# Performance work log

Measured on AMD Instinct MI355X. Metric: run time of the kernel, lower is better.

## Reference

```python
import jax, jax.numpy as jnp
import numpy as np

B, T, N, C, H = 32, 50, 1024, 128, 64


def setup_inputs() -> dict:
    key = jax.random.key(0)
    ks = jax.random.split(key, 5)
    s_ih = 1.0 / np.sqrt(H)
    return {
        "chars": jax.random.normal(ks[0], (B, T, N, C), dtype=jnp.float32),
        "W_ih": jax.random.uniform(ks[1], (3 * H, C), minval=-s_ih, maxval=s_ih, dtype=jnp.float32),
        "W_hh": jax.random.uniform(ks[2], (3 * H, H), minval=-s_ih, maxval=s_ih, dtype=jnp.float32),
        "b_ih": jax.random.uniform(ks[3], (3 * H,), minval=-s_ih, maxval=s_ih, dtype=jnp.float32),
        "b_hh": jax.random.uniform(ks[4], (3 * H,), minval=-s_ih, maxval=s_ih, dtype=jnp.float32),
    }


def _gru_scan(chars, W_ih, W_hh, b_ih, b_hh):
    b, t, n, c = chars.shape
    h_dim = W_hh.shape[1]
    # (B,T,N,C) -> (T, B*N, C): every (batch, stock) pair is an independent sequence
    x = jnp.transpose(chars, (1, 0, 2, 3)).reshape(t, b * n, c)
    # precompute input projections for all steps: (T, B*N, 3H)
    gi = jnp.einsum("tbc,gc->tbg", x, W_ih) + b_ih

    def step(h, gi_t):
        gh = h @ W_hh.T + b_hh                      # (B*N, 3H)
        i_r, i_z, i_n = jnp.split(gi_t, 3, axis=-1)
        h_r, h_z, h_n = jnp.split(gh, 3, axis=-1)
        r = jax.nn.sigmoid(i_r + h_r)
        z = jax.nn.sigmoid(i_z + h_z)
        nn_ = jnp.tanh(i_n + r * h_n)
        h_new = (1.0 - z) * nn_ + z * h
        return h_new, None

    h0 = jnp.zeros((b * n, h_dim), dtype=chars.dtype)
    h_final, _ = jax.lax.scan(step, h0, gi)
    return h_final.reshape(b, n, h_dim)


def reference(chars, W_ih, W_hh, b_ih, b_hh):
    return _gru_scan(chars, W_ih, W_hh, b_ih, b_hh)
```

## Files before the change

kernel.cpp:

```cpp
#include <hip/hip_runtime.h>


typedef _Float16 half8 __attribute__((ext_vector_type(8)));
typedef float f32x16 __attribute__((ext_vector_type(16)));

constexpr int T_ = 50, N_ = 1024, C_ = 128, H_ = 64;
constexpr int WIH_OFF = 0;
constexpr int H_OFF   = 49152;
constexpr int LDS_BYTES = 81920;

__global__ void prep_weights(const float* __restrict__ Wih, const float* __restrict__ Whh,
                             _Float16* __restrict__ w16) {
  int i = blockIdx.x * 256 + threadIdx.x;
  if (i < 192 * 128) w16[i] = (_Float16)Wih[i];
  if (i < 192 * 64)  w16[24576 + i] = (_Float16)Whh[i];
}

__device__ __forceinline__ float sigm(float x) {
  return __builtin_amdgcn_rcpf(1.f + __expf(-x));
}

__global__ __launch_bounds__(256, 1) void gru_mfma32(
    const float* __restrict__ x, const _Float16* __restrict__ w16,
    const float* __restrict__ bih, const float* __restrict__ bhh,
    float* __restrict__ out)
{
  __shared__ __align__(16) char lds[LDS_BYTES];
  const int tid = threadIdx.x;

  {
    const _Float16* wih = w16;
#pragma unroll
    for (int rep = 0; rep < 12; ++rep) {
      int i = tid + rep * 256;
      int row = i >> 4, gr = i & 15;
      uint32_t byte = (uint32_t)row * 256 + (uint32_t)((gr ^ (row & 15)) << 4);
      *(half8*)(lds + WIH_OFF + byte) = *(const half8*)(wih + i * 8);
    }
    half8 zz = {};
#pragma unroll
    for (int rep = 0; rep < 8; ++rep)
      *(half8*)(lds + H_OFF + tid * 128 + rep * 16) = zz;
  }
  __syncthreads();

  const int wv = tid >> 6, lane = tid & 63;
  const int c32 = lane & 31, hf = lane >> 5;
  const int sw15 = c32 & 15;
  const uint32_t hbase = H_OFF + wv * 8192;
  const int gseq0 = blockIdx.x * 128 + wv * 32;
  const int b = gseq0 >> 10, n0 = gseq0 & (N_ - 1);

  const _Float16* whh = w16 + 24576;
  half8 wf[6][4];
#pragma unroll
  for (int ct = 0; ct < 6; ++ct)
#pragma unroll
    for (int ks = 0; ks < 4; ++ks)
      wf[ct][ks] = *(const half8*)(whh + (ct * 32 + c32) * 64 + ks * 16 + hf * 8);

  float br[2], bz[2], bin_[2], bhn_[2];
#pragma unroll
  for (int jj = 0; jj < 2; ++jj) {
    int j = jj * 32 + c32;
    br[jj]   = bih[j] + bhh[j];
    bz[jj]   = bih[64 + j] + bhh[64 + j];
    bin_[jj] = bih[128 + j];
    bhn_[jj] = bhh[128 + j];
  }

  float hr[32];
#pragma unroll
  for (int i = 0; i < 32; ++i) hr[i] = 0.f;

  const float* xlane = x + ((size_t)b * T_ * N_ + n0 + c32) * C_ + hf * 8;
  const size_t stepstride = (size_t)N_ * C_;

#define WIHB(gt, ks) \
  (*(const half8*)(lds + WIH_OFF + (uint32_t)(((gt) * 32 + c32) * 256) + \
                   (uint32_t)(((((ks) * 2 + hf) ^ sw15)) << 4)))
#define MFMA(a, bfrag, acc) __builtin_amdgcn_mfma_f32_32x32x16_f16((a), (bfrag), (acc), 0, 0, 0)

  float4 raw[16];
#pragma unroll
  for (int ks = 0; ks < 8; ++ks) {
    raw[ks * 2]     = *(const float4*)(xlane + ks * 16);
    raw[ks * 2 + 1] = *(const float4*)(xlane + ks * 16 + 4);
  }

  for (int t = 0; t < T_; ++t) {
    half8 xf[8];
#pragma unroll
    for (int ks = 0; ks < 8; ++ks) {
      const float4 lo = raw[ks * 2], hi = raw[ks * 2 + 1];
      half8 v;
      v[0] = (_Float16)lo.x; v[1] = (_Float16)lo.y;
      v[2] = (_Float16)lo.z; v[3] = (_Float16)lo.w;
      v[4] = (_Float16)hi.x; v[5] = (_Float16)hi.y;
      v[6] = (_Float16)hi.z; v[7] = (_Float16)hi.w;
      xf[ks] = v;
    }

    half8 ha[4];
#pragma unroll
    for (int ks = 0; ks < 4; ++ks) {
      uint32_t byte = hbase + (uint32_t)(c32 * 256) + (uint32_t)(((ks * 2 + hf) ^ sw15) << 4);
      ha[ks] = *(const half8*)(lds + byte);
    }

    f32x16 aR0 = {}, aZ0 = {}, aN0 = {}, aH0 = {};
    f32x16 aR1 = {}, aZ1 = {}, aN1 = {}, aH1 = {};

#pragma unroll
    for (int ks = 0; ks < 8; ++ks) aR0 = MFMA(xf[ks], WIHB(0, ks), aR0);
#pragma unroll
    for (int ks = 0; ks < 8; ++ks) aZ0 = MFMA(xf[ks], WIHB(2, ks), aZ0);
#pragma unroll
    for (int ks = 0; ks < 8; ++ks) aN0 = MFMA(xf[ks], WIHB(4, ks), aN0);
#pragma unroll
    for (int ks = 0; ks < 4; ++ks) aR0 = MFMA(ha[ks], wf[0][ks], aR0);
#pragma unroll
    for (int ks = 0; ks < 4; ++ks) aZ0 = MFMA(ha[ks], wf[2][ks], aZ0);
#pragma unroll
    for (int ks = 0; ks < 4; ++ks) aH0 = MFMA(ha[ks], wf[4][ks], aH0);

#pragma unroll
    for (int ks = 0; ks < 8; ++ks) aR1 = MFMA(xf[ks], WIHB(1, ks), aR1);
#pragma unroll
    for (int ks = 0; ks < 8; ++ks) aZ1 = MFMA(xf[ks], WIHB(3, ks), aZ1);
#pragma unroll
    for (int ks = 0; ks < 8; ++ks) aN1 = MFMA(xf[ks], WIHB(5, ks), aN1);

    {
      const int tn = (t + 1 < T_) ? t + 1 : T_ - 1;
      const float* xp = xlane + (size_t)tn * stepstride;
#pragma unroll
      for (int ks = 0; ks < 8; ++ks) {
        raw[ks * 2]     = *(const float4*)(xp + ks * 16);
        raw[ks * 2 + 1] = *(const float4*)(xp + ks * 16 + 4);
      }
    }

#pragma unroll
    for (int ks = 0; ks < 4; ++ks) aR1 = MFMA(ha[ks], wf[1][ks], aR1);
#pragma unroll
    for (int ks = 0; ks < 4; ++ks) aZ1 = MFMA(ha[ks], wf[3][ks], aZ1);
#pragma unroll
    for (int ks = 0; ks < 4; ++ks) aH1 = MFMA(ha[ks], wf[5][ks], aH1);

#pragma unroll
    for (int rg = 0; rg < 16; ++rg) {
      const int seq = (rg & 3) + 8 * (rg >> 2) + 4 * hf;
      const float r = sigm(aR0[rg] + br[0]);
      const float z = sigm(aZ0[rg] + bz[0]);
      const float np = aN0[rg] + bin_[0] + r * (aH0[rg] + bhn_[0]);
      const float nn = 1.f - 2.f * __builtin_amdgcn_rcpf(__expf(2.f * np) + 1.f);
      const float hn = (1.f - z) * nn + z * hr[rg];
      hr[rg] = hn;
      const uint32_t gr = (uint32_t)((0 * 4 + (c32 >> 3)) ^ (seq & 15));
      const uint32_t byte = hbase + (uint32_t)(seq * 256) + (gr << 4) + (uint32_t)((c32 * 2) & 15);
      *(_Float16*)(lds + byte) = (_Float16)hn;
    }
#pragma unroll
    for (int rg = 0; rg < 16; ++rg) {
      const int seq = (rg & 3) + 8 * (rg >> 2) + 4 * hf;
      const float r = sigm(aR1[rg] + br[1]);
      const float z = sigm(aZ1[rg] + bz[1]);
      const float np = aN1[rg] + bin_[1] + r * (aH1[rg] + bhn_[1]);
      const float nn = 1.f - 2.f * __builtin_amdgcn_rcpf(__expf(2.f * np) + 1.f);
      const float hn = (1.f - z) * nn + z * hr[16 + rg];
      hr[16 + rg] = hn;
      const uint32_t gr = (uint32_t)((1 * 4 + (c32 >> 3)) ^ (seq & 15));
      const uint32_t byte = hbase + (uint32_t)(seq * 256) + (gr << 4) + (uint32_t)((c32 * 2) & 15);
      *(_Float16*)(lds + byte) = (_Float16)hn;
    }
  }

#pragma unroll
  for (int jj = 0; jj < 2; ++jj)
#pragma unroll
    for (int rg = 0; rg < 16; ++rg) {
      const int seq = (rg & 3) + 8 * (rg >> 2) + 4 * hf;
      out[(size_t)(gseq0 + seq) * H_ + jj * 32 + c32] = hr[jj * 16 + rg];
    }
#undef WIHB
#undef MFMA
}

extern "C" void kernel_launch(void* const* d_in, const int* in_sizes, int n_in,
                              void* d_out, int out_size, void* d_ws, size_t ws_size,
                              hipStream_t stream) {
  const float* chars = (const float*)d_in[0];
  const float* Wih   = (const float*)d_in[1];
  const float* Whh   = (const float*)d_in[2];
  const float* bih   = (const float*)d_in[3];
  const float* bhh   = (const float*)d_in[4];

  _Float16* w16 = (_Float16*)d_ws;

  prep_weights<<<144, 256, 0, stream>>>(Wih, Whh, w16);
  gru_mfma32<<<256, 256, 0, stream>>>(chars, w16, bih, bhh, (float*)d_out);
}
```

Measured before the change: 231.7 us.

## Split GRU hidden dim across wave pairs with LDS-staged inputs and weights

Doubles the block to 512 threads so each pair of waves shares 32 sequences, with each wave computing half of the hidden units. Each timestep's input tile is converted to fp16 once, written to LDS and read back as MFMA operands. The W_hh fragments move from registers into a swizzled LDS region. The aim is more waves per CU to hide MFMA and load latency, plus lower register pressure. The cost is two block-wide barriers per timestep and extra LDS traffic, and the larger LDS footprint may cap residency at one block per CU despite the launch bounds.

```diff
diff --git a/kernel.cpp b/kernel.cpp
--- a/kernel.cpp
+++ b/kernel.cpp
@@ -5,9 +5,11 @@
 typedef float f32x16 __attribute__((ext_vector_type(16)));
 
 constexpr int T_ = 50, N_ = 1024, C_ = 128, H_ = 64;
-constexpr int WIH_OFF = 0;
-constexpr int H_OFF   = 49152;
-constexpr int LDS_BYTES = 81920;
+constexpr uint32_t WIH_OFF = 0;
+constexpr uint32_t WHH_OFF = 49152;
+constexpr uint32_t XT_OFF  = 73728;
+constexpr uint32_t HT_OFF  = 106496;
+constexpr int LDS_BYTES = 122880;
 
 __global__ void prep_weights(const float* __restrict__ Wih, const float* __restrict__ Whh,
                              _Float16* __restrict__ w16) {
@@ -20,7 +22,7 @@
   return __builtin_amdgcn_rcpf(1.f + __expf(-x));
 }
 
-__global__ __launch_bounds__(256, 1) void gru_mfma32(
+__global__ __launch_bounds__(512, 2) void gru_pair(
     const float* __restrict__ x, const _Float16* __restrict__ w16,
     const float* __restrict__ bih, const float* __restrict__ bhh,
     float* __restrict__ out)
@@ -30,160 +32,136 @@
 
   {
     const _Float16* wih = w16;
+    const _Float16* whh = w16 + 24576;
 #pragma unroll
-    for (int rep = 0; rep < 12; ++rep) {
-      int i = tid + rep * 256;
+    for (int rep = 0; rep < 6; ++rep) {
+      int i = tid + rep * 512;
       int row = i >> 4, gr = i & 15;
       uint32_t byte = (uint32_t)row * 256 + (uint32_t)((gr ^ (row & 15)) << 4);
       *(half8*)(lds + WIH_OFF + byte) = *(const half8*)(wih + i * 8);
     }
+#pragma unroll
+    for (int rep = 0; rep < 3; ++rep) {
+      int i = tid + rep * 512;
+      int row = i >> 3, gr = i & 7;
+      uint32_t byte = (uint32_t)row * 128 + (uint32_t)((gr ^ (row & 7)) << 4);
+      *(half8*)(lds + WHH_OFF + byte) = *(const half8*)(whh + i * 8);
+    }
     half8 zz = {};
-#pragma unroll
-    for (int rep = 0; rep < 8; ++rep)
-      *(half8*)(lds + H_OFF + tid * 128 + rep * 16) = zz;
+    *(half8*)(lds + HT_OFF + tid * 32)      = zz;
+    *(half8*)(lds + HT_OFF + tid * 32 + 16) = zz;
   }
   __syncthreads();
 
   const int wv = tid >> 6, lane = tid & 63;
   const int c32 = lane & 31, hf = lane >> 5;
-  const int sw15 = c32 & 15;
-  const uint32_t hbase = H_OFF + wv * 8192;
-  const int gseq0 = blockIdx.x * 128 + wv * 32;
-  const int b = gseq0 >> 10, n0 = gseq0 & (N_ - 1);
+  const int gl = wv >> 1, jj = wv & 1;
+  const int seq0 = blockIdx.x * 128 + gl * 32;
+  const int b = seq0 >> 10, n0 = seq0 & (N_ - 1);
+  const uint32_t xt = XT_OFF + (uint32_t)gl * 8192;
+  const uint32_t ht = HT_OFF + (uint32_t)gl * 4096;
+  const int j = jj * 32 + c32;
+  const int sw15 = c32 & 15, sw7 = c32 & 7;
 
-  const _Float16* whh = w16 + 24576;
-  half8 wf[6][4];
+  const float br  = bih[j] + bhh[j];
+  const float bz  = bih[64 + j] + bhh[64 + j];
+  const float bin_ = bih[128 + j];
+  const float bhn_ = bhh[128 + j];
+
+  float hr[16];
 #pragma unroll
-  for (int ct = 0; ct < 6; ++ct)
-#pragma unroll
-    for (int ks = 0; ks < 4; ++ks)
-      wf[ct][ks] = *(const half8*)(whh + (ct * 32 + c32) * 64 + ks * 16 + hf * 8);
+  for (int i = 0; i < 16; ++i) hr[i] = 0.f;
 
-  float br[2], bz[2], bin_[2], bhn_[2];
-#pragma unroll
-  for (int jj = 0; jj < 2; ++jj) {
-    int j = jj * 32 + c32;
-    br[jj]   = bih[j] + bhh[j];
-    bz[jj]   = bih[64 + j] + bhh[64 + j];
-    bin_[jj] = bih[128 + j];
-    bhn_[jj] = bhh[128 + j];
-  }
-
-  float hr[32];
-#pragma unroll
-  for (int i = 0; i < 32; ++i) hr[i] = 0.f;
-
-  const float* xlane = x + ((size_t)b * T_ * N_ + n0 + c32) * C_ + hf * 8;
+  const int tp = jj * 64 + lane;
+  const int xseq = tp >> 2, xk0 = (tp & 3) * 32;
+  const float* xptr = x + ((size_t)b * T_ * N_ + n0 + xseq) * C_ + xk0;
   const size_t stepstride = (size_t)N_ * C_;
 
-#define WIHB(gt, ks) \
-  (*(const half8*)(lds + WIH_OFF + (uint32_t)(((gt) * 32 + c32) * 256) + \
-                   (uint32_t)(((((ks) * 2 + hf) ^ sw15)) << 4)))
-#define MFMA(a, bfrag, acc) __builtin_amdgcn_mfma_f32_32x32x16_f16((a), (bfrag), (acc), 0, 0, 0)
+#define WIHB(gate, ks) \
+  (*(const half8*)(lds + WIH_OFF + (uint32_t)(((gate) * 64 + j) * 256) + \
+                   (uint32_t)((((ks) * 2 + hf) ^ sw15) << 4)))
+#define WHHB(gate, ks) \
+  (*(const half8*)(lds + WHH_OFF + (uint32_t)(((gate) * 64 + j) * 128) + \
+                   (uint32_t)((((ks) * 2 + hf) ^ sw7) << 4)))
+#define MFMA(a, bf, acc) __builtin_amdgcn_mfma_f32_32x32x16_f16((a), (bf), (acc), 0, 0, 0)
 
-  float4 raw[16];
+  float4 raw[8];
 #pragma unroll
-  for (int ks = 0; ks < 8; ++ks) {
-    raw[ks * 2]     = *(const float4*)(xlane + ks * 16);
-    raw[ks * 2 + 1] = *(const float4*)(xlane + ks * 16 + 4);
-  }
+  for (int l = 0; l < 8; ++l) raw[l] = *(const float4*)(xptr + l * 4);
 
   for (int t = 0; t < T_; ++t) {
-    half8 xf[8];
 #pragma unroll
-    for (int ks = 0; ks < 8; ++ks) {
-      const float4 lo = raw[ks * 2], hi = raw[ks * 2 + 1];
+    for (int q = 0; q < 4; ++q) {
+      const float4 lo = raw[2 * q], hi = raw[2 * q + 1];
       half8 v;
       v[0] = (_Float16)lo.x; v[1] = (_Float16)lo.y;
       v[2] = (_Float16)lo.z; v[3] = (_Float16)lo.w;
       v[4] = (_Float16)hi.x; v[5] = (_Float16)hi.y;
       v[6] = (_Float16)hi.z; v[7] = (_Float16)hi.w;
-      xf[ks] = v;
+      const uint32_t gj = (uint32_t)((tp & 3) * 4 + q);
+      const uint32_t byte = xt + (uint32_t)xseq * 256 + ((gj ^ (uint32_t)(xseq & 15)) << 4);
+      *(half8*)(lds + byte) = v;
     }
+    __syncthreads();
 
+    half8 xa[8];
+#pragma unroll
+    for (int ks = 0; ks < 8; ++ks)
+      xa[ks] = *(const half8*)(lds + xt + (uint32_t)c32 * 256 +
+                               (uint32_t)(((ks * 2 + hf) ^ sw15) << 4));
     half8 ha[4];
 #pragma unroll
-    for (int ks = 0; ks < 4; ++ks) {
-      uint32_t byte = hbase + (uint32_t)(c32 * 256) + (uint32_t)(((ks * 2 + hf) ^ sw15) << 4);
-      ha[ks] = *(const half8*)(lds + byte);
-    }
+    for (int ks = 0; ks < 4; ++ks)
+      ha[ks] = *(const half8*)(lds + ht + (uint32_t)c32 * 128 +
+                               (uint32_t)(((ks * 2 + hf) ^ sw7) << 4));
+    __syncthreads();
 
-    f32x16 aR0 = {}, aZ0 = {}, aN0 = {}, aH0 = {};
-    f32x16 aR1 = {}, aZ1 = {}, aN1 = {}, aH1 = {};
+    f32x16 aR = {}, aZ = {}, aN = {}, aH = {};
 
 #pragma unroll
-    for (int ks = 0; ks < 8; ++ks) aR0 = MFMA(xf[ks], WIHB(0, ks), aR0);
-#pragma unroll
-    for (int ks = 0; ks < 8; ++ks) aZ0 = MFMA(xf[ks], WIHB(2, ks), aZ0);
-#pragma unroll
-    for (int ks = 0; ks < 8; ++ks) aN0 = MFMA(xf[ks], WIHB(4, ks), aN0);
-#pragma unroll
-    for (int ks = 0; ks < 4; ++ks) aR0 = MFMA(ha[ks], wf[0][ks], aR0);
-#pragma unroll
-    for (int ks = 0; ks < 4; ++ks) aZ0 = MFMA(ha[ks], wf[2][ks], aZ0);
-#pragma unroll
-    for (int ks = 0; ks < 4; ++ks) aH0 = MFMA(ha[ks], wf[4][ks], aH0);
-
-#pragma unroll
-    for (int ks = 0; ks < 8; ++ks) aR1 = MFMA(xf[ks], WIHB(1, ks), aR1);
-#pragma unroll
-    for (int ks = 0; ks < 8; ++ks) aZ1 = MFMA(xf[ks], WIHB(3, ks), aZ1);
-#pragma unroll
-    for (int ks = 0; ks < 8; ++ks) aN1 = MFMA(xf[ks], WIHB(5, ks), aN1);
+    for (int ks = 0; ks < 8; ++ks) {
+      aR = MFMA(xa[ks], WIHB(0, ks), aR);
+      aZ = MFMA(xa[ks], WIHB(1, ks), aZ);
+      aN = MFMA(xa[ks], WIHB(2, ks), aN);
+    }
 
     {
       const int tn = (t + 1 < T_) ? t + 1 : T_ - 1;
-      const float* xp = xlane + (size_t)tn * stepstride;
+      const float* xp = xptr + (size_t)tn * stepstride;
 #pragma unroll
-      for (int ks = 0; ks < 8; ++ks) {
-        raw[ks * 2]     = *(const float4*)(xp + ks * 16);
-        raw[ks * 2 + 1] = *(const float4*)(xp + ks * 16 + 4);
-      }
+      for (int l = 0; l < 8; ++l) raw[l] = *(const float4*)(xp + l * 4);
     }
 
 #pragma unroll
-    for (int ks = 0; ks < 4; ++ks) aR1 = MFMA(ha[ks], wf[1][ks], aR1);
-#pragma unroll
-    for (int ks = 0; ks < 4; ++ks) aZ1 = MFMA(ha[ks], wf[3][ks], aZ1);
-#pragma unroll
-    for (int ks = 0; ks < 4; ++ks) aH1 = MFMA(ha[ks], wf[5][ks], aH1);
+    for (int ks = 0; ks < 4; ++ks) {
+      aR = MFMA(ha[ks], WHHB(0, ks), aR);
+      aZ = MFMA(ha[ks], WHHB(1, ks), aZ);
+      aH = MFMA(ha[ks], WHHB(2, ks), aH);
+    }
 
 #pragma unroll
     for (int rg = 0; rg < 16; ++rg) {
       const int seq = (rg & 3) + 8 * (rg >> 2) + 4 * hf;
-      const float r = sigm(aR0[rg] + br[0]);
-      const float z = sigm(aZ0[rg] + bz[0]);
-      const float np = aN0[rg] + bin_[0] + r * (aH0[rg] + bhn_[0]);
+      const float r = sigm(aR[rg] + br);
+      const float z = sigm(aZ[rg] + bz);
+      const float np = aN[rg] + bin_ + r * (aH[rg] + bhn_);
       const float nn = 1.f - 2.f * __builtin_amdgcn_rcpf(__expf(2.f * np) + 1.f);
       const float hn = (1.f - z) * nn + z * hr[rg];
       hr[rg] = hn;
-      const uint32_t gr = (uint32_t)((0 * 4 + (c32 >> 3)) ^ (seq & 15));
-      const uint32_t byte = hbase + (uint32_t)(seq * 256) + (gr << 4) + (uint32_t)((c32 * 2) & 15);
-      *(_Float16*)(lds + byte) = (_Float16)hn;
-    }
-#pragma unroll
-    for (int rg = 0; rg < 16; ++rg) {
-      const int seq = (rg & 3) + 8 * (rg >> 2) + 4 * hf;
-      const float r = sigm(aR1[rg] + br[1]);
-      const float z = sigm(aZ1[rg] + bz[1]);
-      const float np = aN1[rg] + bin_[1] + r * (aH1[rg] + bhn_[1]);
-      const float nn = 1.f - 2.f * __builtin_amdgcn_rcpf(__expf(2.f * np) + 1.f);
-      const float hn = (1.f - z) * nn + z * hr[16 + rg];
-      hr[16 + rg] = hn;
-      const uint32_t gr = (uint32_t)((1 * 4 + (c32 >> 3)) ^ (seq & 15));
-      const uint32_t byte = hbase + (uint32_t)(seq * 256) + (gr << 4) + (uint32_t)((c32 * 2) & 15);
+      const uint32_t gj = (uint32_t)(jj * 4 + (c32 >> 3));
+      const uint32_t byte = ht + (uint32_t)seq * 128 +
+                            ((gj ^ (uint32_t)(seq & 7)) << 4) + (uint32_t)((c32 & 7) * 2);
       *(_Float16*)(lds + byte) = (_Float16)hn;
     }
   }
 
 #pragma unroll
-  for (int jj = 0; jj < 2; ++jj)
-#pragma unroll
-    for (int rg = 0; rg < 16; ++rg) {
-      const int seq = (rg & 3) + 8 * (rg >> 2) + 4 * hf;
-      out[(size_t)(gseq0 + seq) * H_ + jj * 32 + c32] = hr[jj * 16 + rg];
-    }
+  for (int rg = 0; rg < 16; ++rg) {
+    const int seq = (rg & 3) + 8 * (rg >> 2) + 4 * hf;
+    out[(size_t)(seq0 + seq) * H_ + j] = hr[rg];
+  }
 #undef WIHB
+#undef WHHB
 #undef MFMA
 }
 
@@ -198,6 +176,6 @@
 
   _Float16* w16 = (_Float16*)d_ws;
 
-  prep_weights<<<144, 256, 0, stream>>>(Wih, Whh, w16);
-  gru_mfma32<<<256, 256, 0, stream>>>(chars, w16, bih, bhh, (float*)d_out);
+  prep_weights<<<96, 256, 0, stream>>>(Wih, Whh, w16);
+  gru_pair<<<256, 512, 0, stream>>>(chars, w16, bih, bhh, (float*)d_out);
 }
```

Result: slower. 258.7 us (+11.6%).
